# Optimization experiments

Hardware: AMD Instinct MI355X
Metric: run time of the kernel (lower is better)

The kernel has to match this reference:

```python
import jax, jax.numpy as jnp
import numpy as np

DN = ('NCHW', 'OIHW', 'NCHW')

def conv2d(x, w, b, stride, pad):
    y = jax.lax.conv_general_dilated(x, w, (stride, stride), ((pad, pad), (pad, pad)), dimension_numbers=DN)
    return y + b[None, :, None, None]

def convt2d(x, w, b):
    # torch ConvTranspose2d(k=4, stride=2, padding=1); torch weight layout [Cin, Cout, kH, kW]
    wf = jnp.flip(w, (2, 3)).transpose(1, 0, 2, 3)  # -> [Cout, Cin, kH, kW]
    y = jax.lax.conv_general_dilated(x, wf, (1, 1), ((2, 2), (2, 2)), lhs_dilation=(2, 2), dimension_numbers=DN)
    return y + b[None, :, None, None]

def setup_inputs() -> dict:
    key = jax.random.key(0)
    ks = jax.random.split(key, 20)
    Hc, E, K = 128, 256, 8192
    s = lambda k, shape, fan: jax.random.normal(k, shape, jnp.float32) * (1.0 / np.sqrt(fan))
    inp = {
        'x': jax.random.normal(ks[0], (4, 3, 256, 256), jnp.float32),
        'enc_w1': s(ks[1], (Hc, 3, 4, 4), 3 * 16), 'enc_b1': jnp.zeros((Hc,), jnp.float32),
        'enc_w2': s(ks[2], (Hc, Hc, 4, 4), Hc * 16), 'enc_b2': jnp.zeros((Hc,), jnp.float32),
        'enc_w3': s(ks[3], (Hc, Hc, 3, 3), Hc * 9), 'enc_b3': jnp.zeros((Hc,), jnp.float32),
        'qconv_w': s(ks[4], (E, Hc, 1, 1), Hc), 'qconv_b': jnp.zeros((E,), jnp.float32),
        'codebook': jax.random.uniform(ks[5], (K, E), jnp.float32, -1.0 / K, 1.0 / K),
        'pqconv_w': s(ks[6], (Hc, E, 1, 1), E), 'pqconv_b': jnp.zeros((Hc,), jnp.float32),
        'dec_w1': s(ks[7], (Hc, Hc, 3, 3), Hc * 9), 'dec_b1': jnp.zeros((Hc,), jnp.float32),
        'dect_w2': s(ks[8], (Hc, Hc, 4, 4), Hc * 16), 'dect_b2': jnp.zeros((Hc,), jnp.float32),
        'dect_w3': s(ks[9], (Hc, 3, 4, 4), Hc * 16), 'dect_b3': jnp.zeros((3,), jnp.float32),
    }
    return inp

def quantize(z, codebook):
    B, C, H, W = z.shape
    zf = z.transpose(0, 2, 3, 1).reshape(-1, C)  # [N, C]
    d = (jnp.sum(zf * zf, axis=1, keepdims=True)
         + jnp.sum(codebook * codebook, axis=1)
         - 2.0 * zf @ codebook.T)  # [N, K]
    indices = jnp.argmin(d, axis=1)
    quant = codebook[indices].reshape(B, H, W, C).transpose(0, 3, 1, 2)
    commit_loss = jnp.mean((jax.lax.stop_gradient(quant) - z) ** 2)
    quant = z + jax.lax.stop_gradient(quant - z)  # straight-through
    return quant, indices, commit_loss

def reference(x, enc_w1, enc_b1, enc_w2, enc_b2, enc_w3, enc_b3, qconv_w, qconv_b,
              codebook, pqconv_w, pqconv_b, dec_w1, dec_b1, dect_w2, dect_b2, dect_w3, dect_b3):
    h = jax.nn.relu(conv2d(x, enc_w1, enc_b1, 2, 1))
    h = jax.nn.relu(conv2d(h, enc_w2, enc_b2, 2, 1))
    h = conv2d(h, enc_w3, enc_b3, 1, 1)
    h = conv2d(h, qconv_w, qconv_b, 1, 0)
    quant, indices, commit_loss = quantize(h, codebook)
    q = conv2d(quant, pqconv_w, pqconv_b, 1, 0)
    d = jax.nn.relu(conv2d(q, dec_w1, dec_b1, 1, 1))
    d = jax.nn.relu(convt2d(d, dect_w2, dect_b2))
    recon = convt2d(d, dect_w3, dect_b3)
    return recon, commit_loss, indices
```

## Files before the change

kernel.cpp:

```cpp
#include <hip/hip_runtime.h>

#define OFF_A     ((size_t)0)
#define OFF_BINFO ((size_t)8388608)
#define OFF_B     ((size_t)34611200)
#define OFF_C     ((size_t)43532288)
#define OFF_D     ((size_t)52453376)
#define OFF_E     ((size_t)69230592)
#define OFF_ZN    ((size_t)81813504)
#define OFF_CN    ((size_t)81879040)
#define OFF_IDX   ((size_t)81911808)
#define OFF_ACC   ((size_t)81977344)
#define OFF_WR2   ((size_t)81977600)
#define OFF_WHD1  ((size_t)82501888)
#define OFF_WR3   ((size_t)83026176)
#define OFF_QWT   ((size_t)83050752)
#define OFF_WD2   ((size_t)83181824)
#define OFF_WD3   ((size_t)85278976)
#define OFF_WD1   ((size_t)86458624)

#define VQ_MARGIN 1.2e-4f
#define LDSS 40

typedef __attribute__((ext_vector_type(8))) _Float16 f16x8;
typedef __attribute__((ext_vector_type(4))) float f32x4;

__device__ __forceinline__ unsigned fkey(float f) {
  unsigned u = __float_as_uint(f);
  return (u & 0x80000000u) ? ~u : (u | 0x80000000u);
}
__device__ __forceinline__ float funkey(unsigned k) {
  unsigned u = (k & 0x80000000u) ? (k ^ 0x80000000u) : ~k;
  return __uint_as_float(u);
}
__device__ __forceinline__ void padzero_img(float* base, int S, int t) {
  for (int e = t; e < 4 * S - 4; e += 256) {
    int rr, cc;
    if (e < S) { rr = 0; cc = e; }
    else if (e < 2 * S) { rr = S - 1; cc = e - S; }
    else { rr = ((e - 2 * S) >> 1) + 1; cc = (e & 1) ? (S - 1) : 0; }
    base[rr * S + cc] = 0.0f;
  }
}
__device__ __forceinline__ void padzero_img_h(_Float16* base, int S, int t) {
  for (int e = t; e < 4 * S - 4; e += 256) {
    int rr, cc;
    if (e < S) { rr = 0; cc = e; }
    else if (e < 2 * S) { rr = S - 1; cc = e - S; }
    else { rr = ((e - 2 * S) >> 1) + 1; cc = (e & 1) ? (S - 1) : 0; }
    base[rr * S + cc] = (_Float16)0.0f;
  }
}

__global__ __launch_bounds__(256) void prep_k(
    const float* __restrict__ dtw2, _Float16* __restrict__ wh2,
    const float* __restrict__ dtw3, float* __restrict__ wr3,
    const float* __restrict__ qw,   float* __restrict__ qwT,
    const float* __restrict__ ew2,  double* __restrict__ wd2,
    const float* __restrict__ ew3,  double* __restrict__ wd3,
    const float* __restrict__ ew1,  double* __restrict__ wd1,
    const float* __restrict__ dw1,  _Float16* __restrict__ whd1,
    float* __restrict__ xpad, float* __restrict__ h1p, float* __restrict__ h2p) {
  int b = blockIdx.x, t = threadIdx.x;
  if (b < 256) {
    int tid = b * 256 + t;
    int ci = tid & 127, co = (tid >> 7) & 127, cls = tid >> 14;
    int kh0 = 1 - (cls >> 1), kw0 = 1 - (cls & 1);
    const float* s = dtw2 + ((size_t)ci * 128 + co) * 16;
    _Float16* d = wh2 + (size_t)tid * 4;
    float d0 = s[kh0 * 4 + kw0];       float d1v = s[kh0 * 4 + kw0 + 2];
    float d2v = s[(kh0 + 2) * 4 + kw0]; float d3v = s[(kh0 + 2) * 4 + kw0 + 2];
    d[0] = (_Float16)d1v; d[1] = (_Float16)d0;
    d[2] = (_Float16)d3v; d[3] = (_Float16)d2v;
  } else if (b < 262) {
    int tid = (b - 256) * 256 + t;
    if (tid < 1536) {
      int ci = tid & 127, co = (tid >> 7) % 3, cls = tid / 384;
      int kh0 = 1 - (cls >> 1), kw0 = 1 - (cls & 1);
      const float* s = dtw3 + ((size_t)ci * 3 + co) * 16;
      float* d = wr3 + (size_t)tid * 4;
      d[0] = s[kh0 * 4 + kw0];       d[1] = s[kh0 * 4 + kw0 + 2];
      d[2] = s[(kh0 + 2) * 4 + kw0]; d[3] = s[(kh0 + 2) * 4 + kw0 + 2];
    }
  } else if (b < 390) {
    int tid = (b - 262) * 256 + t;
    int co = tid & 255, ci = tid >> 8;
    qwT[(size_t)ci * 256 + co] = qw[(size_t)co * 128 + ci];
  } else if (b < 1414) {
    int tid = (b - 390) * 256 + t;
    wd2[tid] = (double)ew2[tid];
  } else if (b < 1990) {
    int tid = (b - 1414) * 256 + t;
    wd3[tid] = (double)ew3[tid];
  } else if (b < 2014) {
    int tid = (b - 1990) * 256 + t;
    wd1[tid] = (double)ew1[tid];
  } else if (b < 2026) {
    padzero_img(xpad + (size_t)(b - 2014) * 66564, 258, t);
  } else if (b < 2538) {
    padzero_img(h1p + (size_t)(b - 2026) * 16900, 130, t);
  } else if (b < 3050) {
    padzero_img(h2p + (size_t)(b - 2538) * 4356, 66, t);
  } else {
    int tid = (b - 3050) * 256 + t;
    int co = tid / 1152, k = tid - co * 1152;
    int tap = k >> 7, ci = k & 127;
    whd1[tid] = (_Float16)dw1[((size_t)co * 128 + ci) * 9 + tap];
  }
}

__global__ __launch_bounds__(256) void padx_k(const float* __restrict__ x,
                                              float* __restrict__ xp) {
  int tid = blockIdx.x * 256 + threadIdx.x;
  int wo = tid & 255, ho = (tid >> 8) & 255, c = tid >> 16;
  xp[((size_t)c * 258 + ho + 1) * 258 + wo + 1] = x[tid];
}

__global__ __launch_bounds__(256) void conv1_k(
    const float* __restrict__ xp, const double* __restrict__ wd,
    const float* __restrict__ bias, float* __restrict__ h1p) {
  int b = blockIdx.x;
  int chunk = b & 63, cog = (b >> 6) & 15, n = b >> 10;
  int t = threadIdx.x;
  int wo = t & 127, ho = chunk * 2 + (t >> 7);
  int co0 = cog * 8;
  const float* xb = xp + (size_t)n * 3 * 66564 + (size_t)(2 * ho) * 258 + 2 * wo;
  double acc[8] = {};
  for (int ci = 0; ci < 3; ++ci) {
    const float* xc = xb + (size_t)ci * 66564;
    float cf[16];
#pragma unroll
    for (int kh = 0; kh < 4; ++kh)
#pragma unroll
      for (int kw = 0; kw < 4; ++kw) cf[kh * 4 + kw] = xc[kh * 258 + kw];
    const double* wp = wd + (size_t)co0 * 48 + ci * 16;
#pragma unroll
    for (int tp = 0; tp < 16; ++tp) {
      double xd = (double)cf[tp];
#pragma unroll
      for (int cc = 0; cc < 8; ++cc)
        acc[cc] = fma(xd, wp[(size_t)cc * 48 + tp], acc[cc]);
    }
  }
#pragma unroll
  for (int cc = 0; cc < 8; ++cc) {
    float r = (float)((double)bias[co0 + cc] + acc[cc]);
    h1p[(((size_t)n * 128 + co0 + cc) * 130 + ho + 1) * 130 + wo + 1] = fmaxf(r, 0.0f);
  }
}

__global__ __launch_bounds__(256) void conv2_k(
    const float* __restrict__ h1p, const double* __restrict__ wd,
    const float* __restrict__ bias, float* __restrict__ h2p) {
  int b = blockIdx.x;
  int chunk = b & 15, cog = (b >> 4) & 15, n = b >> 8;
  int t = threadIdx.x;
  int wo = t & 63, ho = chunk * 4 + (t >> 6);
  int co0 = cog * 8;
  const float* xb = h1p + (size_t)n * 128 * 16900 + (size_t)(2 * ho) * 130 + 2 * wo;
  double acc[8] = {};
  for (int ci = 0; ci < 128; ++ci) {
    const float* xc = xb + (size_t)ci * 16900;
    float cf[16];
#pragma unroll
    for (int kh = 0; kh < 4; ++kh) {
      float2 p0 = *(const float2*)(xc + kh * 130);
      float2 p1 = *(const float2*)(xc + kh * 130 + 2);
      cf[kh * 4 + 0] = p0.x; cf[kh * 4 + 1] = p0.y;
      cf[kh * 4 + 2] = p1.x; cf[kh * 4 + 3] = p1.y;
    }
    const double* wp = wd + (size_t)co0 * 2048 + ci * 16;
#pragma unroll
    for (int tp = 0; tp < 16; ++tp) {
      double xd = (double)cf[tp];
#pragma unroll
      for (int cc = 0; cc < 8; ++cc)
        acc[cc] = fma(xd, wp[(size_t)cc * 2048 + tp], acc[cc]);
    }
  }
#pragma unroll
  for (int cc = 0; cc < 8; ++cc) {
    float r = (float)((double)bias[co0 + cc] + acc[cc]);
    h2p[(((size_t)n * 128 + co0 + cc) * 66 + ho + 1) * 66 + wo + 1] = fmaxf(r, 0.0f);
  }
}

__global__ __launch_bounds__(256) void conv3_k(
    const float* __restrict__ h2p, const double* __restrict__ wd,
    const float* __restrict__ bias, float* __restrict__ h3) {
  int b = blockIdx.x;
  int chunk = b & 15, cog = (b >> 4) & 15, n = b >> 8;
  int t = threadIdx.x;
  int wo = t & 63, ho = chunk * 4 + (t >> 6);
  int co0 = cog * 8;
  const float* xb = h2p + (size_t)n * 128 * 4356 + (size_t)ho * 66 + wo;
  double acc[8] = {};
  for (int ci = 0; ci < 128; ++ci) {
    const float* xc = xb + (size_t)ci * 4356;
    float cf[9];
#pragma unroll
    for (int kh = 0; kh < 3; ++kh)
#pragma unroll
      for (int kw = 0; kw < 3; ++kw) cf[kh * 3 + kw] = xc[kh * 66 + kw];
    const double* wp = wd + (size_t)co0 * 1152 + ci * 9;
#pragma unroll
    for (int tp = 0; tp < 9; ++tp) {
      double xd = (double)cf[tp];
#pragma unroll
      for (int cc = 0; cc < 8; ++cc)
        acc[cc] = fma(xd, wp[(size_t)cc * 1152 + tp], acc[cc]);
    }
  }
#pragma unroll
  for (int cc = 0; cc < 8; ++cc)
    h3[(((size_t)n * 128 + co0 + cc) << 12) + (ho << 6) + wo] =
        (float)((double)bias[co0 + cc] + acc[cc]);
}

__global__ __launch_bounds__(256) void qconv_z_k(
    const float* __restrict__ h3, const float* __restrict__ wT,
    const float* __restrict__ bias, float* __restrict__ zf,
    _Float16* __restrict__ Ap, float* __restrict__ znb) {
  __shared__ double wsum[4];
  int p  = blockIdx.x;
  int co = threadIdx.x;
  int n  = p >> 12;
  int hw = p & 4095;
  const float* xp = h3 + ((size_t)n * 128) * 4096 + hw;
  double a[4] = {0.0, 0.0, 0.0, 0.0};
  for (int ci = 0; ci < 128; ci += 4) {
#pragma unroll
    for (int u = 0; u < 4; ++u) {
      float xv = xp[(size_t)(ci + u) * 4096];
      a[u] = fma((double)xv, (double)wT[(size_t)(ci + u) * 256 + co], a[u]);
    }
  }
  double acc = (double)bias[co] + ((a[0] + a[1]) + (a[2] + a[3]));
  float zv = (float)acc;
  zf[(size_t)p * 256 + co] = zv;
  Ap[(size_t)p * 256 + co] = (_Float16)zv;
  float xx = zv * zv;
  double s = (double)xx;
#pragma unroll
  for (int off = 32; off > 0; off >>= 1) s += __shfl_down(s, off, 64);
  if ((co & 63) == 0) wsum[co >> 6] = s;
  __syncthreads();
  if (co == 0) znb[p] = (float)((wsum[0] + wsum[1]) + (wsum[2] + wsum[3]));
}

__global__ __launch_bounds__(256) void cbprep_k(
    const float* __restrict__ cb, _Float16* __restrict__ Bp,
    float* __restrict__ cnb) {
  __shared__ double wsum[4];
  int k = blockIdx.x, t = threadIdx.x;
  float c = cb[(size_t)k * 256 + t];
  Bp[(size_t)k * 256 + t] = (_Float16)(c * 512.0f);
  float xx = c * c;
  double s = (double)xx;
#pragma unroll
  for (int off = 32; off > 0; off >>= 1) s += __shfl_down(s, off, 64);
  if ((t & 63) == 0) wsum[t >> 6] = s;
  __syncthreads();
  if (t == 0) cnb[k] = (float)((wsum[0] + wsum[1]) + (wsum[2] + wsum[3]));
}

__global__ __launch_bounds__(256, 2) void vq_gemm_k(
    const _Float16* __restrict__ Ah, const _Float16* __restrict__ Bh,
    const float* __restrict__ cnArr, int4* __restrict__ binfo) {
  __shared__ __align__(16) _Float16 As[128 * LDSS];
  __shared__ __align__(16) _Float16 Bs[128 * LDSS];
  __shared__ unsigned loc[128];
  __shared__ int cnt_sh[128];
  __shared__ int cand_sh[128][2];
  const int t = threadIdx.x;
  const int w = t >> 6, L = t & 63;
  const int mb = blockIdx.x >> 6;
  const int nb = blockIdx.x & 63;
  const int m0 = mb << 7, n0 = nb << 7;
  if (t < 128) { loc[t] = 0xFFFFFFFFu; cnt_sh[t] = 0; }
  f32x4 acc[4][4] = {};
  const int wr = (w >> 1) << 6, wc = (w & 1) << 6;
  const int srow = L >> 2, kg = L & 3;
  const int q = L >> 4, ln = L & 15;
  for (int kk = 0; kk < 256; kk += 32) {
    __syncthreads();
#pragma unroll
    for (int c = 0; c < 2; ++c) {
      const int row = (w << 5) + (c << 4) + srow;
      const f16x8 av = *(const f16x8*)(Ah + (size_t)(m0 + row) * 256 + kk + kg * 8);
      *(f16x8*)(&As[row * LDSS + kg * 8]) = av;
      const f16x8 bv = *(const f16x8*)(Bh + (size_t)(n0 + row) * 256 + kk + kg * 8);
      *(f16x8*)(&Bs[row * LDSS + kg * 8]) = bv;
    }
    __syncthreads();
    f16x8 af[4], bf[4];
#pragma unroll
    for (int i = 0; i < 4; ++i)
      af[i] = *(const f16x8*)(&As[(wr + 16 * i + ln) * LDSS + q * 8]);
#pragma unroll
    for (int j = 0; j < 4; ++j)
      bf[j] = *(const f16x8*)(&Bs[(wc + 16 * j + ln) * LDSS + q * 8]);
#pragma unroll
    for (int i = 0; i < 4; ++i)
#pragma unroll
      for (int j = 0; j < 4; ++j)
        acc[i][j] = __builtin_amdgcn_mfma_f32_16x16x32_f16(af[i], bf[j], acc[i][j], 0, 0, 0);
  }
  float cnv[4];
#pragma unroll
  for (int j = 0; j < 4; ++j) cnv[j] = cnArr[n0 + wc + 16 * j + ln];
#pragma unroll
  for (int i = 0; i < 4; ++i)
#pragma unroll
    for (int r = 0; r < 4; ++r) {
      float mn = 3.4e38f;
#pragma unroll
      for (int j = 0; j < 4; ++j)
        mn = fminf(mn, fmaf(-0.00390625f, acc[i][j][r], cnv[j]));
#pragma unroll
      for (int s = 1; s < 16; s <<= 1)
        mn = fminf(mn, __shfl_xor(mn, s, 64));
      if (ln == 0) atomicMin(&loc[wr + 16 * i + 4 * q + r], fkey(mn));
    }
  __syncthreads();
#pragma unroll
  for (int i = 0; i < 4; ++i)
#pragma unroll
    for (int r = 0; r < 4; ++r) {
      const int rib = wr + 16 * i + 4 * q + r;
      const float thr = funkey(loc[rib]) + VQ_MARGIN;
#pragma unroll
      for (int j = 0; j < 4; ++j) {
        float s = fmaf(-0.00390625f, acc[i][j][r], cnv[j]);
        if (s <= thr) {
          int slot = atomicAdd(&cnt_sh[rib], 1);
          if (slot < 2) cand_sh[rib][slot] = n0 + wc + 16 * j + ln;
        }
      }
    }
  __syncthreads();
  if (t < 128) {
    int4 v;
    v.x = cnt_sh[t];
    v.y = cand_sh[t][0];
    v.z = cand_sh[t][1];
    v.w = (int)__float_as_uint(funkey(loc[t]));
    binfo[(size_t)(m0 + t) * 64 + nb] = v;
  }
}

__global__ __launch_bounds__(256) void vq_phase3_k(
    const float* __restrict__ zf, const float* __restrict__ cb,
    const float* __restrict__ znArr, const float* __restrict__ cnArr,
    const int4* __restrict__ binfo, int* __restrict__ idxOut,
    float* __restrict__ accum) {
  if (blockIdx.x == 0 && threadIdx.x == 0) *accum = 0.0f;
  const int lane = threadIdx.x & 63;
  const int r = blockIdx.x * 4 + (threadIdx.x >> 6);
  const float* zr = zf + (size_t)r * 256;
  double z4[4];
#pragma unroll
  for (int j = 0; j < 4; ++j) z4[j] = (double)zr[lane + (j << 6)];
  const float znr = znArr[r];
  int4 b = binfo[(size_t)r * 64 + lane];
  float bv = __uint_as_float((unsigned)b.w);
  float m = bv;
#pragma unroll
  for (int off = 32; off > 0; off >>= 1) m = fminf(m, __shfl_down(m, off, 64));
  m = __shfl(m, 0, 64);
  const float thr = m + VQ_MARGIN;
  unsigned long long mask = __ballot(bv <= thr);
  float bestd = 3.4e38f;
  int bestk = 0x7fffffff;
  while (mask) {
    const int nb = (int)__builtin_ctzll(mask);
    mask &= mask - 1;
    const int c  = __shfl(b.x, nb, 64);
    const int k0 = __shfl(b.y, nb, 64);
    const int k1 = __shfl(b.z, nb, 64);
    const int nsc = (c <= 2) ? c : 128;
    for (int s2 = 0; s2 < nsc; ++s2) {
      const int k = (c <= 2) ? (s2 == 0 ? k0 : k1) : (nb * 128 + s2);
      const float* ck = cb + (size_t)k * 256;
      double p = 0.0;
#pragma unroll
      for (int j = 0; j < 4; ++j)
        p = fma(z4[j], (double)ck[lane + (j << 6)], p);
#pragma unroll
      for (int off = 32; off > 0; off >>= 1) p += __shfl_down(p, off, 64);
      if (lane == 0) {
        float mm2 = (float)(2.0 * p);
        float t1 = znr + cnArr[k];
        float d = t1 - mm2;
        if (d < bestd || (d == bestd && k < bestk)) { bestd = d; bestk = k; }
      }
    }
  }
  if (lane == 0) idxOut[r] = bestk;
}

__global__ __launch_bounds__(256) void commit_k(
    const float* __restrict__ zf, const float* __restrict__ cb,
    const int* __restrict__ idxArr, float* __restrict__ accum,
    float* __restrict__ outIdxF) {
  __shared__ float wsum[4];
  const int p = blockIdx.x;
  const int t = threadIdx.x;
  const int k = idxArr[p];
  float d = cb[(size_t)k * 256 + t] - zf[(size_t)p * 256 + t];
  float v = d * d;
#pragma unroll
  for (int off = 32; off > 0; off >>= 1) v += __shfl_down(v, off, 64);
  if ((t & 63) == 0) wsum[t >> 6] = v;
  __syncthreads();
  if (t == 0) {
    atomicAdd(accum, wsum[0] + wsum[1] + wsum[2] + wsum[3]);
    outIdxF[p] = (float)k;
  }
}

__global__ __launch_bounds__(256) void pc_k(const float* __restrict__ cb,
                                            const float* __restrict__ pw,
                                            float* __restrict__ PC) {
  int tid = blockIdx.x * 256 + threadIdx.x;
  int co = tid & 127, k = tid >> 7;
  const float* c = cb + (size_t)k * 256;
  const float* w = pw + (size_t)co * 256;
  float a0 = 0.0f, a1 = 0.0f, a2 = 0.0f, a3 = 0.0f;
  for (int ci = 0; ci < 256; ci += 4) {
    a0 = fmaf(c[ci], w[ci], a0);
    a1 = fmaf(c[ci + 1], w[ci + 1], a1);
    a2 = fmaf(c[ci + 2], w[ci + 2], a2);
    a3 = fmaf(c[ci + 3], w[ci + 3], a3);
  }
  PC[tid] = (a0 + a1) + (a2 + a3);
}

__global__ __launch_bounds__(256) void padzero_dec_k(
    _Float16* __restrict__ qH, _Float16* __restrict__ d1pH,
    _Float16* __restrict__ d2pH) {
  int b = blockIdx.x, t = threadIdx.x;
  if (b < 512)       padzero_img_h(qH + (size_t)b * 4356, 66, t);
  else if (b < 1024) padzero_img_h(d1pH + (size_t)(b - 512) * 4356, 66, t);
  else               padzero_img_h(d2pH + (size_t)(b - 1024) * 16900, 130, t);
}

__global__ __launch_bounds__(256) void gather_pc_k(
    const float* __restrict__ PC, const int* __restrict__ idxArr,
    const float* __restrict__ pb, _Float16* __restrict__ qH) {
  int tid = blockIdx.x * 256 + threadIdx.x;
  int hw = tid & 4095;
  int co = (tid >> 12) & 127;
  int n  = tid >> 19;
  int p  = (n << 12) + hw;
  int h = hw >> 6, w2 = hw & 63;
  qH[(((size_t)n * 128 + co) * 66 + h + 1) * 66 + w2 + 1] =
      (_Float16)(PC[(size_t)idxArr[p] * 128 + co] + pb[co]);
}

__global__ __launch_bounds__(256) void dconv1_k(
    const _Float16* __restrict__ qH, const _Float16* __restrict__ wa,
    const float* __restrict__ bias, _Float16* __restrict__ d1pH) {
  int b = blockIdx.x;
  int ho = b & 63, cog = (b >> 6) & 7, n = b >> 9;
  int t = threadIdx.x;
  int wv = t >> 6, l = t & 63;
  int q = l >> 4, ln = l & 15;
  int wo0 = wv << 4;
  const unsigned short* qb = (const unsigned short*)qH + (size_t)n * 128 * 4356;
  const _Float16* ap = wa + (size_t)(cog * 16 + ln) * 1152 + q * 8;
  f32x4 acc = {0.0f, 0.0f, 0.0f, 0.0f};
#pragma unroll
  for (int s = 0; s < 36; ++s) {
    const int tap = s >> 2, dh = tap / 3, dw = tap % 3;
    const int cig = ((s & 3) << 5) + (q << 3);
    const unsigned short* bp =
        qb + (size_t)cig * 4356 + (ho + dh) * 66 + wo0 + ln + dw;
    unsigned v0 = bp[0],        v1 = bp[4356];
    unsigned v2 = bp[2 * 4356], v3 = bp[3 * 4356];
    unsigned v4 = bp[4 * 4356], v5 = bp[5 * 4356];
    unsigned v6 = bp[6 * 4356], v7 = bp[7 * 4356];
    union { unsigned u[4]; f16x8 h; } bb;
    bb.u[0] = v0 | (v1 << 16);
    bb.u[1] = v2 | (v3 << 16);
    bb.u[2] = v4 | (v5 << 16);
    bb.u[3] = v6 | (v7 << 16);
    const f16x8 af = *(const f16x8*)(ap + s * 32);
    acc = __builtin_amdgcn_mfma_f32_16x16x32_f16(af, bb.h, acc, 0, 0, 0);
  }
#pragma unroll
  for (int r = 0; r < 4; ++r) {
    int co = (cog << 4) + (q << 2) + r;
    d1pH[(((size_t)n * 128 + co) * 66 + ho + 1) * 66 + wo0 + ln + 1] =
        (_Float16)fmaxf(bias[co] + acc[r], 0.0f);
  }
}

__global__ __launch_bounds__(256) void convt2_k(
    const _Float16* __restrict__ xh, const _Float16* __restrict__ wh,
    const float* __restrict__ bias, _Float16* __restrict__ y) {
  int b = blockIdx.x;
  int i = b & 63, cog = (b >> 6) & 7, cls = (b >> 9) & 3, n = b >> 11;
  int cph = cls >> 1, cpw = cls & 1;
  int t = threadIdx.x;
  int wv = t >> 6, l = t & 63;
  int q = l >> 4, ln = l & 15;
  int wb = (wv << 4) + ln;
  int co0 = cog << 4;
  int r0 = i + 1 + cph, r1 = r0 - 1;
  int c1 = wb + cpw;
  int o0 = r0 * 66 + c1, o1 = r1 * 66 + c1;
  const unsigned short* xb =
      (const unsigned short*)xh + (size_t)n * 128 * 4356 + (size_t)(q * 2) * 4356;
  const _Float16* ap = wh + (size_t)(cls * 128 + co0 + ln) * 512 + q * 8;
  f32x4 acc = {0.0f, 0.0f, 0.0f, 0.0f};
  for (int s = 0; s < 16; ++s) {
    const unsigned short* pa = xb + (size_t)(s * 8) * 4356;
    const unsigned short* pb2 = pa + 4356;
    unsigned v0 = pa[o0], v1 = pa[o0 + 1];
    unsigned v2 = pa[o1], v3 = pa[o1 + 1];
    unsigned v4 = pb2[o0], v5 = pb2[o0 + 1];
    unsigned v6 = pb2[o1], v7 = pb2[o1 + 1];
    union { unsigned u[4]; f16x8 h; } bb;
    bb.u[0] = v0 | (v1 << 16);
    bb.u[1] = v2 | (v3 << 16);
    bb.u[2] = v4 | (v5 << 16);
    bb.u[3] = v6 | (v7 << 16);
    const f16x8 af = *(const f16x8*)(ap + s * 32);
    acc = __builtin_amdgcn_mfma_f32_16x16x32_f16(af, bb.h, acc, 0, 0, 0);
  }
  int ho = 2 * i + cph, wo = 2 * wb + cpw;
#pragma unroll
  for (int r = 0; r < 4; ++r) {
    int co = co0 + q * 4 + r;
    y[(((size_t)n * 128 + co) * 130 + ho + 1) * 130 + wo + 1] =
        (_Float16)fmaxf(bias[co] + acc[r], 0.0f);
  }
}

__global__ __launch_bounds__(256) void convt3_k(
    const _Float16* __restrict__ xh, const float* __restrict__ wr,
    const float* __restrict__ bias, float* __restrict__ y,
    const float* __restrict__ accum, float* __restrict__ outLoss) {
  int b = blockIdx.x;
  if (b == 0 && threadIdx.x == 0) *outLoss = *accum * (1.0f / 4194304.0f);
  int chunk = b & 63, cls = (b >> 6) & 3, n = b >> 8;
  int cph = cls >> 1, cpw = cls & 1;
  int t = threadIdx.x;
  int wb = t & 127, i = chunk * 2 + (t >> 7);
  int ho = 2 * i + cph, wo = 2 * wb + cpw;
  int r0 = i + 1 + cph, r1 = r0 - 1;
  int c0 = wb + 1 + cpw, c1 = c0 - 1;
  const _Float16* xb = xh + (size_t)n * 128 * 16900;
  float acc[3] = {0.0f, 0.0f, 0.0f};
  for (int ci = 0; ci < 128; ++ci) {
    const _Float16* xc = xb + (size_t)ci * 16900;
    float x00 = (float)xc[r0 * 130 + c0], x01 = (float)xc[r0 * 130 + c1];
    float x10 = (float)xc[r1 * 130 + c0], x11 = (float)xc[r1 * 130 + c1];
#pragma unroll
    for (int cc = 0; cc < 3; ++cc) {
      const float* w4 = wr + (((size_t)cls * 3 + cc) * 128 + ci) * 4;
      acc[cc] = fmaf(x00, w4[0], acc[cc]);
      acc[cc] = fmaf(x01, w4[1], acc[cc]);
      acc[cc] = fmaf(x10, w4[2], acc[cc]);
      acc[cc] = fmaf(x11, w4[3], acc[cc]);
    }
  }
#pragma unroll
  for (int cc = 0; cc < 3; ++cc)
    y[(((size_t)n * 3 + cc) << 16) + (ho << 8) + wo] = bias[cc] + acc[cc];
}

extern "C" void kernel_launch(void* const* d_in, const int* in_sizes, int n_in,
                              void* d_out, int out_size, void* d_ws, size_t ws_size,
                              hipStream_t stream) {
  const float* x    = (const float*)d_in[0];
  const float* ew1  = (const float*)d_in[1];
  const float* eb1  = (const float*)d_in[2];
  const float* ew2  = (const float*)d_in[3];
  const float* eb2  = (const float*)d_in[4];
  const float* ew3  = (const float*)d_in[5];
  const float* eb3  = (const float*)d_in[6];
  const float* qw   = (const float*)d_in[7];
  const float* qb   = (const float*)d_in[8];
  const float* cb   = (const float*)d_in[9];
  const float* pw   = (const float*)d_in[10];
  const float* pb   = (const float*)d_in[11];
  const float* dw1  = (const float*)d_in[12];
  const float* db1  = (const float*)d_in[13];
  const float* dtw2 = (const float*)d_in[14];
  const float* dtb2 = (const float*)d_in[15];
  const float* dtw3 = (const float*)d_in[16];
  const float* dtb3 = (const float*)d_in[17];

  char* wsb = (char*)d_ws;
  float*    h1p  = (float*)(wsb + OFF_A);
  _Float16* Ap   = (_Float16*)(wsb + OFF_A);
  int4*     binfo= (int4*)(wsb + OFF_BINFO);
  _Float16* d2pH = (_Float16*)(wsb + OFF_A);
  float*    h2p  = (float*)(wsb + OFF_B);
  _Float16* qH   = (_Float16*)(wsb + OFF_B);
  float*    xpad = (float*)(wsb + OFF_C);
  float*    h3   = (float*)(wsb + OFF_C);
  _Float16* d1pH = (_Float16*)(wsb + OFF_C);
  float*    zff  = (float*)(wsb + OFF_D);
  _Float16* Bp   = (_Float16*)(wsb + OFF_E);
  float*    PC   = (float*)(wsb + OFF_E);
  float*    znb  = (float*)(wsb + OFF_ZN);
  float*    cnb  = (float*)(wsb + OFF_CN);
  int*      idxb = (int*)(wsb + OFF_IDX);
  float*    accum= (float*)(wsb + OFF_ACC);
  _Float16* wh2  = (_Float16*)(wsb + OFF_WR2);
  _Float16* whd1 = (_Float16*)(wsb + OFF_WHD1);
  float*    wr3  = (float*)(wsb + OFF_WR3);
  float*    qwT  = (float*)(wsb + OFF_QWT);
  double*   wd2  = (double*)(wsb + OFF_WD2);
  double*   wd3  = (double*)(wsb + OFF_WD3);
  double*   wd1  = (double*)(wsb + OFF_WD1);

  float* out      = (float*)d_out;
  float* outLoss  = out + 786432;
  float* outIdxF  = out + 786433;

  hipLaunchKernelGGL(prep_k, dim3(3626), dim3(256), 0, stream,
                     dtw2, wh2, dtw3, wr3, qw, qwT, ew2, wd2, ew3, wd3,
                     ew1, wd1, dw1, whd1, xpad, h1p, h2p);

  hipLaunchKernelGGL(padx_k,    dim3(3072),  dim3(256), 0, stream, x, xpad);
  hipLaunchKernelGGL(conv1_k,   dim3(4096),  dim3(256), 0, stream, xpad, wd1, eb1, h1p);
  hipLaunchKernelGGL(conv2_k,   dim3(1024),  dim3(256), 0, stream, h1p, wd2, eb2, h2p);
  hipLaunchKernelGGL(conv3_k,   dim3(1024),  dim3(256), 0, stream, h2p, wd3, eb3, h3);
  hipLaunchKernelGGL(qconv_z_k, dim3(16384), dim3(256), 0, stream, h3, qwT, qb, zff, Ap, znb);

  hipLaunchKernelGGL(cbprep_k,    dim3(8192),  dim3(256), 0, stream, cb, Bp, cnb);
  hipLaunchKernelGGL(vq_gemm_k,   dim3(8192),  dim3(256), 0, stream, Ap, Bp, cnb, binfo);
  hipLaunchKernelGGL(vq_phase3_k, dim3(4096),  dim3(256), 0, stream, zff, cb, znb, cnb, binfo, idxb, accum);
  hipLaunchKernelGGL(commit_k,    dim3(16384), dim3(256), 0, stream, zff, cb, idxb, accum, outIdxF);

  hipLaunchKernelGGL(pc_k,          dim3(4096), dim3(256), 0, stream, cb, pw, PC);
  hipLaunchKernelGGL(padzero_dec_k, dim3(1536), dim3(256), 0, stream, qH, d1pH, d2pH);
  hipLaunchKernelGGL(gather_pc_k,   dim3(8192), dim3(256), 0, stream, PC, idxb, pb, qH);
  hipLaunchKernelGGL(dconv1_k,      dim3(2048), dim3(256), 0, stream, qH, whd1, db1, d1pH);
  hipLaunchKernelGGL(convt2_k,      dim3(8192), dim3(256), 0, stream, d1pH, wh2, dtb2, d2pH);
  hipLaunchKernelGGL(convt3_k,      dim3(1024), dim3(256), 0, stream, d2pH, wr3, dtb3, out, accum, outLoss);
}
```

Measured before the change: 1.338 ms.

## Split conv2 and conv3 input channels in two with combine kernels

```diff
diff --git a/kernel.cpp b/kernel.cpp
--- a/kernel.cpp
+++ b/kernel.cpp
@@ -20,6 +20,7 @@
 
 #define VQ_MARGIN 1.2e-4f
 #define LDSS 40
+#define P_HALF ((size_t)2097152)
 
 typedef __attribute__((ext_vector_type(8))) _Float16 f16x8;
 typedef __attribute__((ext_vector_type(4))) float f32x4;
@@ -150,15 +151,18 @@
 
 __global__ __launch_bounds__(256) void conv2_k(
     const float* __restrict__ h1p, const double* __restrict__ wd,
-    const float* __restrict__ bias, float* __restrict__ h2p) {
+    double* __restrict__ P2) {
   int b = blockIdx.x;
-  int chunk = b & 15, cog = (b >> 4) & 15, n = b >> 8;
+  int half = b >> 10;
+  int r = b & 1023;
+  int chunk = r & 15, cog = (r >> 4) & 15, n = r >> 8;
   int t = threadIdx.x;
   int wo = t & 63, ho = chunk * 4 + (t >> 6);
   int co0 = cog * 8;
   const float* xb = h1p + (size_t)n * 128 * 16900 + (size_t)(2 * ho) * 130 + 2 * wo;
   double acc[8] = {};
-  for (int ci = 0; ci < 128; ++ci) {
+  const int ci0 = half << 6;
+  for (int ci = ci0; ci < ci0 + 64; ++ci) {
     const float* xc = xb + (size_t)ci * 16900;
     float cf[16];
 #pragma unroll
@@ -177,24 +181,41 @@
         acc[cc] = fma(xd, wp[(size_t)cc * 2048 + tp], acc[cc]);
     }
   }
-#pragma unroll
-  for (int cc = 0; cc < 8; ++cc) {
-    float r = (float)((double)bias[co0 + cc] + acc[cc]);
-    h2p[(((size_t)n * 128 + co0 + cc) * 66 + ho + 1) * 66 + wo + 1] = fmaxf(r, 0.0f);
-  }
+  double* pp = P2 + (size_t)half * P_HALF
+             + ((((size_t)n * 16 + cog) * 16 + chunk) << 11) + t;
+#pragma unroll
+  for (int cc = 0; cc < 8; ++cc) pp[cc << 8] = acc[cc];
+}
+
+__global__ __launch_bounds__(256) void combine2_k(
+    const double* __restrict__ P2, const float* __restrict__ bias,
+    float* __restrict__ h2p) {
+  int idx = blockIdx.x * 256 + threadIdx.x;
+  int wo = idx & 63, hor = (idx >> 6) & 3, cc = (idx >> 8) & 7;
+  int chunk = (idx >> 11) & 15, cog = (idx >> 15) & 15, n = (idx >> 19) & 3;
+  int tl = hor * 64 + wo;
+  size_t base = ((((size_t)n * 16 + cog) * 16 + chunk) << 11) + (cc << 8) + tl;
+  double p0 = P2[base];
+  double p1 = P2[P_HALF + base];
+  int ho = chunk * 4 + hor, co = cog * 8 + cc;
+  float r = (float)((double)bias[co] + (p0 + p1));
+  h2p[(((size_t)n * 128 + co) * 66 + ho + 1) * 66 + wo + 1] = fmaxf(r, 0.0f);
 }
 
 __global__ __launch_bounds__(256) void conv3_k(
     const float* __restrict__ h2p, const double* __restrict__ wd,
-    const float* __restrict__ bias, float* __restrict__ h3) {
+    double* __restrict__ P3) {
   int b = blockIdx.x;
-  int chunk = b & 15, cog = (b >> 4) & 15, n = b >> 8;
+  int half = b >> 10;
+  int r = b & 1023;
+  int chunk = r & 15, cog = (r >> 4) & 15, n = r >> 8;
   int t = threadIdx.x;
   int wo = t & 63, ho = chunk * 4 + (t >> 6);
   int co0 = cog * 8;
   const float* xb = h2p + (size_t)n * 128 * 4356 + (size_t)ho * 66 + wo;
   double acc[8] = {};
-  for (int ci = 0; ci < 128; ++ci) {
+  const int ci0 = half << 6;
+  for (int ci = ci0; ci < ci0 + 64; ++ci) {
     const float* xc = xb + (size_t)ci * 4356;
     float cf[9];
 #pragma unroll
@@ -210,10 +231,25 @@
         acc[cc] = fma(xd, wp[(size_t)cc * 1152 + tp], acc[cc]);
     }
   }
-#pragma unroll
-  for (int cc = 0; cc < 8; ++cc)
-    h3[(((size_t)n * 128 + co0 + cc) << 12) + (ho << 6) + wo] =
-        (float)((double)bias[co0 + cc] + acc[cc]);
+  double* pp = P3 + (size_t)half * P_HALF
+             + ((((size_t)n * 16 + cog) * 16 + chunk) << 11) + t;
+#pragma unroll
+  for (int cc = 0; cc < 8; ++cc) pp[cc << 8] = acc[cc];
+}
+
+__global__ __launch_bounds__(256) void combine3_k(
+    const double* __restrict__ P3, const float* __restrict__ bias,
+    float* __restrict__ h3) {
+  int idx = blockIdx.x * 256 + threadIdx.x;
+  int wo = idx & 63, hor = (idx >> 6) & 3, cc = (idx >> 8) & 7;
+  int chunk = (idx >> 11) & 15, cog = (idx >> 15) & 15, n = (idx >> 19) & 3;
+  int tl = hor * 64 + wo;
+  size_t base = ((((size_t)n * 16 + cog) * 16 + chunk) << 11) + (cc << 8) + tl;
+  double p0 = P3[base];
+  double p1 = P3[P_HALF + base];
+  int ho = chunk * 4 + hor, co = cog * 8 + cc;
+  h3[(((size_t)n * 128 + co) << 12) + (ho << 6) + wo] =
+      (float)((double)bias[co] + (p0 + p1));
 }
 
 __global__ __launch_bounds__(256) void qconv_z_k(
@@ -594,12 +630,14 @@
 
   char* wsb = (char*)d_ws;
   float*    h1p  = (float*)(wsb + OFF_A);
+  double*   P3   = (double*)(wsb + OFF_A);
   _Float16* Ap   = (_Float16*)(wsb + OFF_A);
   int4*     binfo= (int4*)(wsb + OFF_BINFO);
   _Float16* d2pH = (_Float16*)(wsb + OFF_A);
   float*    h2p  = (float*)(wsb + OFF_B);
   _Float16* qH   = (_Float16*)(wsb + OFF_B);
   float*    xpad = (float*)(wsb + OFF_C);
+  double*   P2   = (double*)(wsb + OFF_C);
   float*    h3   = (float*)(wsb + OFF_C);
   _Float16* d1pH = (_Float16*)(wsb + OFF_C);
   float*    zff  = (float*)(wsb + OFF_D);
@@ -627,8 +665,10 @@
 
   hipLaunchKernelGGL(padx_k,    dim3(3072),  dim3(256), 0, stream, x, xpad);
   hipLaunchKernelGGL(conv1_k,   dim3(4096),  dim3(256), 0, stream, xpad, wd1, eb1, h1p);
-  hipLaunchKernelGGL(conv2_k,   dim3(1024),  dim3(256), 0, stream, h1p, wd2, eb2, h2p);
-  hipLaunchKernelGGL(conv3_k,   dim3(1024),  dim3(256), 0, stream, h2p, wd3, eb3, h3);
+  hipLaunchKernelGGL(conv2_k,   dim3(2048),  dim3(256), 0, stream, h1p, wd2, P2);
+  hipLaunchKernelGGL(combine2_k,dim3(8192),  dim3(256), 0, stream, P2, eb2, h2p);
+  hipLaunchKernelGGL(conv3_k,   dim3(2048),  dim3(256), 0, stream, h2p, wd3, P3);
+  hipLaunchKernelGGL(combine3_k,dim3(8192),  dim3(256), 0, stream, P3, eb3, h3);
   hipLaunchKernelGGL(qconv_z_k, dim3(16384), dim3(256), 0, stream, h3, qwT, qb, zff, Ap, znb);
 
   hipLaunchKernelGGL(cbprep_k,    dim3(8192),  dim3(256), 0, stream, cb, Bp, cnb);
```

After: 1.373 ms. 1.03x slower.
